# Kernel optimization log

Measured on AMD Instinct MI355X. Metric: run time of the kernel, lower is better.

Reference implementation:

```python
import jax, jax.numpy as jnp
import numpy as np

B, C, W, H = 4, 256, 64, 64
CQ = C // 8


def setup_inputs() -> dict:
    key = jax.random.key(0)
    ks = jax.random.split(key, 8)
    s = 1.0 / np.sqrt(C)
    return {
        "x": jax.random.normal(ks[0], (B, C, W, H), dtype=jnp.float32),
        "Wq": jax.random.normal(ks[1], (CQ, C), dtype=jnp.float32) * s,
        "bq": jnp.zeros((CQ,), dtype=jnp.float32),
        "Wk": jax.random.normal(ks[2], (CQ, C), dtype=jnp.float32) * s,
        "bk": jnp.zeros((CQ,), dtype=jnp.float32),
        "Wv": jax.random.normal(ks[3], (C, C), dtype=jnp.float32) * s,
        "bv": jnp.zeros((C,), dtype=jnp.float32),
        "gamma": jnp.zeros((1,), dtype=jnp.float32),
    }


def reference(x, Wq, bq, Wk, bk, Wv, bv, gamma):
    b, c, w, h = x.shape
    n = w * h
    xf = x.reshape(b, c, n)  # [B, C, N] flattened spatial
    # 1x1 convs are channel-wise linear maps
    q = jnp.einsum("dc,bcn->bnd", Wq, xf) + bq  # [B, N, C//8]
    k = jnp.einsum("dc,bcn->bdn", Wk, xf) + bk[None, :, None]  # [B, C//8, N]
    v = jnp.einsum("dc,bcn->bdn", Wv, xf) + bv[None, :, None]  # [B, C, N]
    attn = jax.nn.softmax(jnp.einsum("bnd,bdm->bnm", q, k), axis=-1)  # [B, N, N]
    # out[b, c, n] = sum_m v[b, c, m] * attn[b, n, m]
    out = jnp.einsum("bdm,bnm->bdn", v, attn).reshape(b, c, w, h)
    return gamma[0] * out + x
```

## Files before the change

### kernel.cpp

```cpp
#include <hip/hip_runtime.h>
#include <hip/hip_bf16.h>

#define CC 256
#define NN 4096
#define CQ 32
#define LOG2E 1.4426950408889634f

using short8 = __attribute__((ext_vector_type(8))) short;
using f32x4  = __attribute__((ext_vector_type(4))) float;

static __device__ __forceinline__ short f2bf(float f) {
  __hip_bfloat16 h = __float2bfloat16(f);
  return *reinterpret_cast<short*>(&h);
}

__global__ __launch_bounds__(256) void prep_kernel(
    const float* __restrict__ Wq, const float* __restrict__ Wk,
    const float* __restrict__ Wv, __hip_bfloat16* __restrict__ Wf)
{
  int t = blockIdx.x*256 + threadIdx.x;
  int lane = t & 63, frag = t >> 6;
  int tile = frag >> 3, kc = frag & 7;
  int l15 = lane & 15, quad = lane >> 4;
  int R = tile*16 + l15;
  int k0 = kc*32 + quad*8;
  const float* src;
  if (R < 32)       src = Wq + (size_t)R*CC + k0;
  else if (R < 64)  src = Wk + (size_t)(R-32)*CC + k0;
  else              src = Wv + (size_t)(R-64)*CC + k0;
  float4 a = *(const float4*)(src);
  float4 c = *(const float4*)(src + 4);
  short8 o;
  o[0]=f2bf(a.x); o[1]=f2bf(a.y); o[2]=f2bf(a.z); o[3]=f2bf(a.w);
  o[4]=f2bf(c.x); o[5]=f2bf(c.y); o[6]=f2bf(c.z); o[7]=f2bf(c.w);
  *reinterpret_cast<short8*>(reinterpret_cast<short*>(Wf) + (size_t)t*8) = o;
}

__global__ __launch_bounds__(512, 2) void qkv_kernel(
    const float* __restrict__ x, const __hip_bfloat16* __restrict__ Wf,
    const float* __restrict__ bq, const float* __restrict__ bk,
    const float* __restrict__ bv,
    __hip_bfloat16* __restrict__ qb, __hip_bfloat16* __restrict__ kb,
    __hip_bfloat16* __restrict__ vb)
{
  const int b  = blockIdx.y;
  const int n0 = blockIdx.x * 64;
  const int tid = threadIdx.x;
  const int lane = tid & 63;
  const int w = __builtin_amdgcn_readfirstlane(tid >> 6);
  const int l15 = lane & 15, quad = lane >> 4;

  __shared__ __align__(16) short Xs[64][264];
  __shared__ __align__(16) short Vr[8][16][72];

  const int sn = tid & 63, cg8 = tid >> 6;
  const float* xcol = x + (size_t)b*CC*NN + n0 + sn;
#pragma unroll
  for (int it = 0; it < 4; it++) {
    int cbase = it*64 + cg8*8;
    float v[8];
#pragma unroll
    for (int j = 0; j < 8; j++) v[j] = xcol[(size_t)(cbase + j)*NN];
    short8 sv;
#pragma unroll
    for (int j = 0; j < 8; j++) sv[j] = f2bf(v[j]);
    *reinterpret_cast<short8*>(&Xs[sn][cbase]) = sv;
  }
  __syncthreads();

  const short* wfp = reinterpret_cast<const short*>(Wf);

#define QKV_TILE(T) { \
    const int t_ = (T); \
    short8 Af[8]; \
    _Pragma("unroll") \
    for (int kc = 0; kc < 8; kc++) \
      Af[kc] = *(const short8*)(wfp + ((size_t)(t_*8 + kc)*64 + lane)*8); \
    f32x4 ac0 = {0.f,0.f,0.f,0.f}, ac1 = {0.f,0.f,0.f,0.f}; \
    f32x4 ac2 = {0.f,0.f,0.f,0.f}, ac3 = {0.f,0.f,0.f,0.f}; \
    _Pragma("unroll") \
    for (int kc = 0; kc < 8; kc++) { \
      short8 B0 = *(const short8*)(&Xs[     l15][kc*32 + quad*8]); \
      short8 B1 = *(const short8*)(&Xs[16 + l15][kc*32 + quad*8]); \
      short8 B2 = *(const short8*)(&Xs[32 + l15][kc*32 + quad*8]); \
      short8 B3 = *(const short8*)(&Xs[48 + l15][kc*32 + quad*8]); \
      ac0 = __builtin_amdgcn_mfma_f32_16x16x32_bf16(Af[kc], B0, ac0, 0,0,0); \
      ac1 = __builtin_amdgcn_mfma_f32_16x16x32_bf16(Af[kc], B1, ac1, 0,0,0); \
      ac2 = __builtin_amdgcn_mfma_f32_16x16x32_bf16(Af[kc], B2, ac2, 0,0,0); \
      ac3 = __builtin_amdgcn_mfma_f32_16x16x32_bf16(Af[kc], B3, ac3, 0,0,0); \
    } \
    if (t_ < 2) { \
      int d0 = t_*16; \
      _Pragma("unroll") \
      for (int r = 0; r < 4; r++) { \
        int d = d0 + quad*4 + r; float bb = bq[d]; \
        qb[(size_t)b*NN*CQ + (size_t)(n0      + l15)*CQ + d] = __float2bfloat16(LOG2E*(ac0[r] + bb)); \
        qb[(size_t)b*NN*CQ + (size_t)(n0 + 16 + l15)*CQ + d] = __float2bfloat16(LOG2E*(ac1[r] + bb)); \
        qb[(size_t)b*NN*CQ + (size_t)(n0 + 32 + l15)*CQ + d] = __float2bfloat16(LOG2E*(ac2[r] + bb)); \
        qb[(size_t)b*NN*CQ + (size_t)(n0 + 48 + l15)*CQ + d] = __float2bfloat16(LOG2E*(ac3[r] + bb)); \
      } \
    } else if (t_ < 4) { \
      int d0 = (t_-2)*16; \
      _Pragma("unroll") \
      for (int r = 0; r < 4; r++) { \
        int d = d0 + quad*4 + r; float bb = bk[d]; \
        kb[(size_t)b*NN*CQ + (size_t)(n0      + l15)*CQ + d] = __float2bfloat16(ac0[r] + bb); \
        kb[(size_t)b*NN*CQ + (size_t)(n0 + 16 + l15)*CQ + d] = __float2bfloat16(ac1[r] + bb); \
        kb[(size_t)b*NN*CQ + (size_t)(n0 + 32 + l15)*CQ + d] = __float2bfloat16(ac2[r] + bb); \
        kb[(size_t)b*NN*CQ + (size_t)(n0 + 48 + l15)*CQ + d] = __float2bfloat16(ac3[r] + bb); \
      } \
    } else { \
      int rv0 = (t_-4)*16; \
      _Pragma("unroll") \
      for (int r = 0; r < 4; r++) { \
        float bb = bv[rv0 + quad*4 + r]; \
        Vr[w][quad*4 + r][     l15] = f2bf(ac0[r] + bb); \
        Vr[w][quad*4 + r][16 + l15] = f2bf(ac1[r] + bb); \
        Vr[w][quad*4 + r][32 + l15] = f2bf(ac2[r] + bb); \
        Vr[w][quad*4 + r][48 + l15] = f2bf(ac3[r] + bb); \
      } \
      int row = lane >> 2, cb = (lane & 3)*16; \
      short8 t0 = *(const short8*)(&Vr[w][row][cb]); \
      short8 t1 = *(const short8*)(&Vr[w][row][cb + 8]); \
      *(short8*)(vb + ((size_t)b*CC + rv0 + row)*NN + n0 + cb)     = t0; \
      *(short8*)(vb + ((size_t)b*CC + rv0 + row)*NN + n0 + cb + 8) = t1; \
    } }

  QKV_TILE(2*w);
  QKV_TILE(2*w + 1);
  if (w < 4) { QKV_TILE(16 + w); }
#undef QKV_TILE
}

__global__ __launch_bounds__(512, 2) void attn_kernel(
    const __hip_bfloat16* __restrict__ qb, const __hip_bfloat16* __restrict__ kb,
    const __hip_bfloat16* __restrict__ vb,
    const float* __restrict__ x, const float* __restrict__ gamma,
    float* __restrict__ out)
{
  const int Bk = blockIdx.x;
  const int b = (Bk & 7) >> 1;
  const int n0 = ((Bk >> 3)*2 + (Bk & 1)) * 64;
  const int tid = threadIdx.x;
  const int lane = tid & 63;
  const int w = __builtin_amdgcn_readfirstlane(tid >> 6);
  const int sg = w & 3;
  const int mh = w >> 2;
  const int l15 = lane & 15, quad = lane >> 4;

  __shared__ __align__(16) short Vs[256][72];
  __shared__ __align__(16) short Ps[64][72];
  __shared__ float Lbuf2[2][64];

  const short* qbase = (const short*)qb + (size_t)b*NN*CQ;
  const short* kbase = (const short*)kb + (size_t)b*NN*CQ;
  const short* vbase = (const short*)vb + (size_t)b*CC*NN;

  short8 aq = *(const short8*)(qbase + (size_t)(n0 + sg*16 + l15)*CQ + quad*8);

  const int vr = tid >> 1, sh = tid & 1;

  short8 vf0, vf1, vf2, vf3, kf0, kf1;
#pragma unroll
  for (int j = 0; j < 4; j++) {
    short8 t = *(const short8*)(vbase + (size_t)vr*NN + sh*32 + j*8);
    if (j == 0) vf0 = t; else if (j == 1) vf1 = t; else if (j == 2) vf2 = t; else vf3 = t;
  }
  kf0 = *(const short8*)(kbase + (size_t)(mh*32 +      l15)*CQ + quad*8);
  kf1 = *(const short8*)(kbase + (size_t)(mh*32 + 16 + l15)*CQ + quad*8);
  *(short8*)(&Vs[vr][sh*32 +  0]) = vf0;
  *(short8*)(&Vs[vr][sh*32 +  8]) = vf1;
  *(short8*)(&Vs[vr][sh*32 + 16]) = vf2;
  *(short8*)(&Vs[vr][sh*32 + 24]) = vf3;

  f32x4 acc[4][4];
#pragma unroll
  for (int cg = 0; cg < 4; cg++)
#pragma unroll
    for (int ng = 0; ng < 4; ng++) acc[cg][ng] = (f32x4){0.f,0.f,0.f,0.f};
  float lsum[4] = {0.f,0.f,0.f,0.f};

  __syncthreads();

  for (int T = 0; T < 64; T++) {
    short8 nv0, nv1, nv2, nv3, nk0, nk1;
    if (T < 63) {
      const short* vp = vbase + (size_t)vr*NN + (T+1)*64 + sh*32;
      nv0 = *(const short8*)(vp);
      nv1 = *(const short8*)(vp + 8);
      nv2 = *(const short8*)(vp + 16);
      nv3 = *(const short8*)(vp + 24);
      nk0 = *(const short8*)(kbase + (size_t)((T+1)*64 + mh*32 +      l15)*CQ + quad*8);
      nk1 = *(const short8*)(kbase + (size_t)((T+1)*64 + mh*32 + 16 + l15)*CQ + quad*8);
    }

    f32x4 z = {0.f,0.f,0.f,0.f};
    f32x4 S0 = __builtin_amdgcn_mfma_f32_16x16x32_bf16(aq, kf0, z, 0,0,0);
    f32x4 S1 = __builtin_amdgcn_mfma_f32_16x16x32_bf16(aq, kf1, z, 0,0,0);
#pragma unroll
    for (int r = 0; r < 4; r++) {
      float e0 = __builtin_amdgcn_exp2f(S0[r]);
      float e1 = __builtin_amdgcn_exp2f(S1[r]);
      lsum[r] += e0 + e1;
      Ps[sg*16 + quad*4 + r][mh*32 +      l15] = f2bf(e0);
      Ps[sg*16 + quad*4 + r][mh*32 + 16 + l15] = f2bf(e1);
    }
    __syncthreads();

    short8 ap0 = *(const short8*)(&Ps[     l15][mh*32 + quad*8]);
    short8 ap1 = *(const short8*)(&Ps[16 + l15][mh*32 + quad*8]);
    short8 ap2 = *(const short8*)(&Ps[32 + l15][mh*32 + quad*8]);
    short8 ap3 = *(const short8*)(&Ps[48 + l15][mh*32 + quad*8]);
#pragma unroll
    for (int cg = 0; cg < 4; cg++) {
      short8 av = *(const short8*)(&Vs[sg*64 + cg*16 + l15][mh*32 + quad*8]);
      acc[cg][0] = __builtin_amdgcn_mfma_f32_16x16x32_bf16(av, ap0, acc[cg][0], 0,0,0);
      acc[cg][1] = __builtin_amdgcn_mfma_f32_16x16x32_bf16(av, ap1, acc[cg][1], 0,0,0);
      acc[cg][2] = __builtin_amdgcn_mfma_f32_16x16x32_bf16(av, ap2, acc[cg][2], 0,0,0);
      acc[cg][3] = __builtin_amdgcn_mfma_f32_16x16x32_bf16(av, ap3, acc[cg][3], 0,0,0);
    }
    __syncthreads();

    if (T < 63) {
      *(short8*)(&Vs[vr][sh*32 +  0]) = nv0;
      *(short8*)(&Vs[vr][sh*32 +  8]) = nv1;
      *(short8*)(&Vs[vr][sh*32 + 16]) = nv2;
      *(short8*)(&Vs[vr][sh*32 + 24]) = nv3;
      kf0 = nk0; kf1 = nk1;
    }
  }

#pragma unroll
  for (int r = 0; r < 4; r++) {
    float s = lsum[r];
    s += __shfl_xor(s, 1); s += __shfl_xor(s, 2);
    s += __shfl_xor(s, 4); s += __shfl_xor(s, 8);
    if (l15 == 0) Lbuf2[mh][sg*16 + quad*4 + r] = s;
  }

  float* poolf = reinterpret_cast<float*>(&Vs[0][0]);
  __syncthreads();
#pragma unroll
  for (int g = 0; g < 2; g++) {
    if (mh == 1 && (sg >> 1) == g) {
#pragma unroll
      for (int cg = 0; cg < 4; cg++)
#pragma unroll
        for (int ng = 0; ng < 4; ng++)
#pragma unroll
          for (int r = 0; r < 4; r++)
            poolf[(sg & 1)*4096 + (cg*16 + quad*4 + r)*64 + ng*16 + l15] = acc[cg][ng][r];
    }
    __syncthreads();
    if (mh == 0 && (sg >> 1) == g) {
#pragma unroll
      for (int cg = 0; cg < 4; cg++)
#pragma unroll
        for (int ng = 0; ng < 4; ng++)
#pragma unroll
          for (int r = 0; r < 4; r++)
            acc[cg][ng][r] += poolf[(sg & 1)*4096 + (cg*16 + quad*4 + r)*64 + ng*16 + l15];
    }
    __syncthreads();
  }

  if (mh == 0) {
    const float gm = gamma[0];
    float Lv[4];
#pragma unroll
    for (int ng = 0; ng < 4; ng++)
      Lv[ng] = 1.0f / (Lbuf2[0][ng*16 + l15] + Lbuf2[1][ng*16 + l15]);
#pragma unroll
    for (int cg = 0; cg < 4; cg++) {
#pragma unroll
      for (int ng = 0; ng < 4; ng++) {
#pragma unroll
        for (int r = 0; r < 4; r++) {
          size_t idx = ((size_t)b*CC + sg*64 + cg*16 + quad*4 + r)*NN + n0 + ng*16 + l15;
          out[idx] = gm * acc[cg][ng][r] * Lv[ng] + x[idx];
        }
      }
    }
  }
}

extern "C" void kernel_launch(void* const* d_in, const int* in_sizes, int n_in,
                              void* d_out, int out_size, void* d_ws, size_t ws_size,
                              hipStream_t stream) {
  const float* x     = (const float*)d_in[0];
  const float* Wq    = (const float*)d_in[1];
  const float* bq    = (const float*)d_in[2];
  const float* Wk    = (const float*)d_in[3];
  const float* bk    = (const float*)d_in[4];
  const float* Wv    = (const float*)d_in[5];
  const float* bv    = (const float*)d_in[6];
  const float* gamma = (const float*)d_in[7];
  float* out = (float*)d_out;

  char* ws = (char*)d_ws;
  if (ws_size < (11u << 20)) return;
  __hip_bfloat16* qb = (__hip_bfloat16*)(ws);
  __hip_bfloat16* kb = (__hip_bfloat16*)(ws + (1u << 20));
  __hip_bfloat16* vb = (__hip_bfloat16*)(ws + (2u << 20));
  __hip_bfloat16* Wf = (__hip_bfloat16*)(ws + (10u << 20));

  prep_kernel<<<dim3(40), 256, 0, stream>>>(Wq, Wk, Wv, Wf);
  qkv_kernel<<<dim3(64, 4), 512, 0, stream>>>(x, Wf, bq, bk, bv, qb, kb, vb);
  attn_kernel<<<dim3(256), 512, 0, stream>>>(qb, kb, vb, x, gamma, out);
}
```

Before: 155.6 us.

## Fuse weight conversion into QKV kernel and privatize V tiles per wave

Removes the separate prep kernel so weights are read as fp32 and converted to bf16 inside the QKV kernel, saving one launch. In the attention kernel each wave now loads its own V sub-tile into a private LDS slot, and the P buffer is double-buffered. Together these remove the second block-wide barrier per iteration. The cost is redundant weight conversion in every QKV block and a different, strided global access pattern for V loads.

```diff
diff --git a/kernel.cpp b/kernel.cpp
--- a/kernel.cpp
+++ b/kernel.cpp
@@ -14,32 +14,11 @@
   return *reinterpret_cast<short*>(&h);
 }
 
-__global__ __launch_bounds__(256) void prep_kernel(
-    const float* __restrict__ Wq, const float* __restrict__ Wk,
-    const float* __restrict__ Wv, __hip_bfloat16* __restrict__ Wf)
-{
-  int t = blockIdx.x*256 + threadIdx.x;
-  int lane = t & 63, frag = t >> 6;
-  int tile = frag >> 3, kc = frag & 7;
-  int l15 = lane & 15, quad = lane >> 4;
-  int R = tile*16 + l15;
-  int k0 = kc*32 + quad*8;
-  const float* src;
-  if (R < 32)       src = Wq + (size_t)R*CC + k0;
-  else if (R < 64)  src = Wk + (size_t)(R-32)*CC + k0;
-  else              src = Wv + (size_t)(R-64)*CC + k0;
-  float4 a = *(const float4*)(src);
-  float4 c = *(const float4*)(src + 4);
-  short8 o;
-  o[0]=f2bf(a.x); o[1]=f2bf(a.y); o[2]=f2bf(a.z); o[3]=f2bf(a.w);
-  o[4]=f2bf(c.x); o[5]=f2bf(c.y); o[6]=f2bf(c.z); o[7]=f2bf(c.w);
-  *reinterpret_cast<short8*>(reinterpret_cast<short*>(Wf) + (size_t)t*8) = o;
-}
-
 __global__ __launch_bounds__(512, 2) void qkv_kernel(
-    const float* __restrict__ x, const __hip_bfloat16* __restrict__ Wf,
-    const float* __restrict__ bq, const float* __restrict__ bk,
-    const float* __restrict__ bv,
+    const float* __restrict__ x,
+    const float* __restrict__ Wq, const float* __restrict__ bq,
+    const float* __restrict__ Wk, const float* __restrict__ bk,
+    const float* __restrict__ Wv, const float* __restrict__ bv,
     __hip_bfloat16* __restrict__ qb, __hip_bfloat16* __restrict__ kb,
     __hip_bfloat16* __restrict__ vb)
 {
@@ -68,14 +47,23 @@
   }
   __syncthreads();
 
-  const short* wfp = reinterpret_cast<const short*>(Wf);
-
 #define QKV_TILE(T) { \
     const int t_ = (T); \
+    const float* wr; \
+    { int R = t_*16 + l15; \
+      if (t_ < 2)      wr = Wq + (size_t)R*CC; \
+      else if (t_ < 4) wr = Wk + (size_t)(R-32)*CC; \
+      else             wr = Wv + (size_t)(R-64)*CC; } \
     short8 Af[8]; \
     _Pragma("unroll") \
-    for (int kc = 0; kc < 8; kc++) \
-      Af[kc] = *(const short8*)(wfp + ((size_t)(t_*8 + kc)*64 + lane)*8); \
+    for (int kc = 0; kc < 8; kc++) { \
+      float4 fa = *(const float4*)(wr + kc*32 + quad*8); \
+      float4 fc = *(const float4*)(wr + kc*32 + quad*8 + 4); \
+      short8 o; \
+      o[0]=f2bf(fa.x); o[1]=f2bf(fa.y); o[2]=f2bf(fa.z); o[3]=f2bf(fa.w); \
+      o[4]=f2bf(fc.x); o[5]=f2bf(fc.y); o[6]=f2bf(fc.z); o[7]=f2bf(fc.w); \
+      Af[kc] = o; \
+    } \
     f32x4 ac0 = {0.f,0.f,0.f,0.f}, ac1 = {0.f,0.f,0.f,0.f}; \
     f32x4 ac2 = {0.f,0.f,0.f,0.f}, ac3 = {0.f,0.f,0.f,0.f}; \
     _Pragma("unroll") \
@@ -148,8 +136,8 @@
   const int mh = w >> 2;
   const int l15 = lane & 15, quad = lane >> 4;
 
-  __shared__ __align__(16) short Vs[256][72];
-  __shared__ __align__(16) short Ps[64][72];
+  __shared__ __align__(16) short Vsp[8][64][40];
+  __shared__ __align__(16) short Ps[2][2][64][40];
   __shared__ float Lbuf2[2][64];
 
   const short* qbase = (const short*)qb + (size_t)b*NN*CQ;
@@ -158,20 +146,23 @@
 
   short8 aq = *(const short8*)(qbase + (size_t)(n0 + sg*16 + l15)*CQ + quad*8);
 
-  const int vr = tid >> 1, sh = tid & 1;
-
-  short8 vf0, vf1, vf2, vf3, kf0, kf1;
-#pragma unroll
-  for (int j = 0; j < 4; j++) {
-    short8 t = *(const short8*)(vbase + (size_t)vr*NN + sh*32 + j*8);
-    if (j == 0) vf0 = t; else if (j == 1) vf1 = t; else if (j == 2) vf2 = t; else vf3 = t;
+  const int vrow = lane >> 2, vch = lane & 3;
+  const short* vwave = vbase + (size_t)(sg*64)*NN + mh*32 + vch*8;
+
+  short8 nv0, nv1, nv2, nv3, kf0, kf1, nk0, nk1;
+  {
+    const short* vp = vwave + (size_t)vrow*NN;
+    nv0 = *(const short8*)(vp);
+    nv1 = *(const short8*)(vp + (size_t)16*NN);
+    nv2 = *(const short8*)(vp + (size_t)32*NN);
+    nv3 = *(const short8*)(vp + (size_t)48*NN);
   }
   kf0 = *(const short8*)(kbase + (size_t)(mh*32 +      l15)*CQ + quad*8);
   kf1 = *(const short8*)(kbase + (size_t)(mh*32 + 16 + l15)*CQ + quad*8);
-  *(short8*)(&Vs[vr][sh*32 +  0]) = vf0;
-  *(short8*)(&Vs[vr][sh*32 +  8]) = vf1;
-  *(short8*)(&Vs[vr][sh*32 + 16]) = vf2;
-  *(short8*)(&Vs[vr][sh*32 + 24]) = vf3;
+  *(short8*)(&Vsp[w][vrow     ][vch*8]) = nv0;
+  *(short8*)(&Vsp[w][vrow + 16][vch*8]) = nv1;
+  *(short8*)(&Vsp[w][vrow + 32][vch*8]) = nv2;
+  *(short8*)(&Vsp[w][vrow + 48][vch*8]) = nv3;
 
   f32x4 acc[4][4];
 #pragma unroll
@@ -180,16 +171,13 @@
     for (int ng = 0; ng < 4; ng++) acc[cg][ng] = (f32x4){0.f,0.f,0.f,0.f};
   float lsum[4] = {0.f,0.f,0.f,0.f};
 
-  __syncthreads();
-
   for (int T = 0; T < 64; T++) {
-    short8 nv0, nv1, nv2, nv3, nk0, nk1;
     if (T < 63) {
-      const short* vp = vbase + (size_t)vr*NN + (T+1)*64 + sh*32;
+      const short* vp = vwave + (size_t)vrow*NN + (T+1)*64;
       nv0 = *(const short8*)(vp);
-      nv1 = *(const short8*)(vp + 8);
-      nv2 = *(const short8*)(vp + 16);
-      nv3 = *(const short8*)(vp + 24);
+      nv1 = *(const short8*)(vp + (size_t)16*NN);
+      nv2 = *(const short8*)(vp + (size_t)32*NN);
+      nv3 = *(const short8*)(vp + (size_t)48*NN);
       nk0 = *(const short8*)(kbase + (size_t)((T+1)*64 + mh*32 +      l15)*CQ + quad*8);
       nk1 = *(const short8*)(kbase + (size_t)((T+1)*64 + mh*32 + 16 + l15)*CQ + quad*8);
     }
@@ -197,35 +185,35 @@
     f32x4 z = {0.f,0.f,0.f,0.f};
     f32x4 S0 = __builtin_amdgcn_mfma_f32_16x16x32_bf16(aq, kf0, z, 0,0,0);
     f32x4 S1 = __builtin_amdgcn_mfma_f32_16x16x32_bf16(aq, kf1, z, 0,0,0);
+    const int pb = T & 1;
 #pragma unroll
     for (int r = 0; r < 4; r++) {
       float e0 = __builtin_amdgcn_exp2f(S0[r]);
       float e1 = __builtin_amdgcn_exp2f(S1[r]);
       lsum[r] += e0 + e1;
-      Ps[sg*16 + quad*4 + r][mh*32 +      l15] = f2bf(e0);
-      Ps[sg*16 + quad*4 + r][mh*32 + 16 + l15] = f2bf(e1);
+      Ps[pb][mh][sg*16 + quad*4 + r][     l15] = f2bf(e0);
+      Ps[pb][mh][sg*16 + quad*4 + r][16 + l15] = f2bf(e1);
     }
     __syncthreads();
 
-    short8 ap0 = *(const short8*)(&Ps[     l15][mh*32 + quad*8]);
-    short8 ap1 = *(const short8*)(&Ps[16 + l15][mh*32 + quad*8]);
-    short8 ap2 = *(const short8*)(&Ps[32 + l15][mh*32 + quad*8]);
-    short8 ap3 = *(const short8*)(&Ps[48 + l15][mh*32 + quad*8]);
+    short8 ap0 = *(const short8*)(&Ps[pb][mh][     l15][quad*8]);
+    short8 ap1 = *(const short8*)(&Ps[pb][mh][16 + l15][quad*8]);
+    short8 ap2 = *(const short8*)(&Ps[pb][mh][32 + l15][quad*8]);
+    short8 ap3 = *(const short8*)(&Ps[pb][mh][48 + l15][quad*8]);
 #pragma unroll
     for (int cg = 0; cg < 4; cg++) {
-      short8 av = *(const short8*)(&Vs[sg*64 + cg*16 + l15][mh*32 + quad*8]);
+      short8 av = *(const short8*)(&Vsp[w][cg*16 + l15][quad*8]);
       acc[cg][0] = __builtin_amdgcn_mfma_f32_16x16x32_bf16(av, ap0, acc[cg][0], 0,0,0);
       acc[cg][1] = __builtin_amdgcn_mfma_f32_16x16x32_bf16(av, ap1, acc[cg][1], 0,0,0);
       acc[cg][2] = __builtin_amdgcn_mfma_f32_16x16x32_bf16(av, ap2, acc[cg][2], 0,0,0);
       acc[cg][3] = __builtin_amdgcn_mfma_f32_16x16x32_bf16(av, ap3, acc[cg][3], 0,0,0);
     }
-    __syncthreads();
 
     if (T < 63) {
-      *(short8*)(&Vs[vr][sh*32 +  0]) = nv0;
-      *(short8*)(&Vs[vr][sh*32 +  8]) = nv1;
-      *(short8*)(&Vs[vr][sh*32 + 16]) = nv2;
-      *(short8*)(&Vs[vr][sh*32 + 24]) = nv3;
+      *(short8*)(&Vsp[w][vrow     ][vch*8]) = nv0;
+      *(short8*)(&Vsp[w][vrow + 16][vch*8]) = nv1;
+      *(short8*)(&Vsp[w][vrow + 32][vch*8]) = nv2;
+      *(short8*)(&Vsp[w][vrow + 48][vch*8]) = nv3;
       kf0 = nk0; kf1 = nk1;
     }
   }
@@ -238,7 +226,7 @@
     if (l15 == 0) Lbuf2[mh][sg*16 + quad*4 + r] = s;
   }
 
-  float* poolf = reinterpret_cast<float*>(&Vs[0][0]);
+  float* poolf = reinterpret_cast<float*>(&Vsp[0][0][0]);
   __syncthreads();
 #pragma unroll
   for (int g = 0; g < 2; g++) {
@@ -298,13 +286,11 @@
   float* out = (float*)d_out;
 
   char* ws = (char*)d_ws;
-  if (ws_size < (11u << 20)) return;
+  if (ws_size < (10u << 20)) return;
   __hip_bfloat16* qb = (__hip_bfloat16*)(ws);
   __hip_bfloat16* kb = (__hip_bfloat16*)(ws + (1u << 20));
   __hip_bfloat16* vb = (__hip_bfloat16*)(ws + (2u << 20));
-  __hip_bfloat16* Wf = (__hip_bfloat16*)(ws + (10u << 20));
-
-  prep_kernel<<<dim3(40), 256, 0, stream>>>(Wq, Wk, Wv, Wf);
-  qkv_kernel<<<dim3(64, 4), 512, 0, stream>>>(x, Wf, bq, bk, bv, qb, kb, vb);
+
+  qkv_kernel<<<dim3(64, 4), 512, 0, stream>>>(x, Wq, bq, Wk, bk, Wv, bv, qb, kb, vb);
   attn_kernel<<<dim3(256), 512, 0, stream>>>(qb, kb, vb, x, gamma, out);
 }
```

Result: no change. 156.1 us (+0.4%).
